# Kernel tuning notes

Hardware: AMD Instinct MI355X
Metric: run time of the kernel (lower is better)

The kernel has to match this reference:

```python
import jax, jax.numpy as jnp
import numpy as np

N, E = 50000, 800000
HID, HEADS, EDIM = 64, 4, 3
NEG_SLOPE = 0.2
LN_EPS = 1e-5


def setup_inputs() -> dict:
    key = jax.random.key(0)
    ks = jax.random.split(key, 12)
    h = jax.random.normal(ks[0], (N, HID), dtype=jnp.float32)
    edge_index = jax.random.randint(ks[1], (2, E), 0, N, dtype=jnp.int64)
    edge_attr = jax.random.normal(ks[2], (E, EDIM), dtype=jnp.float32)
    t = jax.random.uniform(ks[3], (1,), dtype=jnp.float32)
    s = 1.0 / np.sqrt(HID)
    W = jax.random.normal(ks[4], (HID, HEADS * HID), dtype=jnp.float32) * s
    att_src = jax.random.normal(ks[5], (1, HEADS, HID), dtype=jnp.float32) * s
    att_dst = jax.random.normal(ks[6], (1, HEADS, HID), dtype=jnp.float32) * s
    W_edge = jax.random.normal(ks[7], (EDIM, HEADS * HID), dtype=jnp.float32) * s
    att_edge = jax.random.normal(ks[8], (1, HEADS, HID), dtype=jnp.float32) * s
    bias = jnp.zeros((HID,), dtype=jnp.float32)
    ln_gamma = jnp.ones((HID,), dtype=jnp.float32)
    ln_beta = jnp.zeros((HID,), dtype=jnp.float32)
    return {"t": t, "h": h, "edge_index": edge_index, "edge_attr": edge_attr,
            "W": W, "att_src": att_src, "att_dst": att_dst, "W_edge": W_edge,
            "att_edge": att_edge, "bias": bias, "ln_gamma": ln_gamma, "ln_beta": ln_beta}


def reference(t, h, edge_index, edge_attr, W, att_src, att_dst, W_edge, att_edge, bias, ln_gamma, ln_beta):
    # GATConv (PyG, edge_dim>0, add_self_loops=False, concat=False, eval mode)
    x = (h @ W).reshape(N, HEADS, HID)                     # [N,H,C]
    a_src = (x * att_src).sum(-1)                          # [N,H]
    a_dst = (x * att_dst).sum(-1)                          # [N,H]
    e = (edge_attr @ W_edge).reshape(E, HEADS, HID)        # [E,H,C]
    a_edge = (e * att_edge).sum(-1)                        # [E,H]
    src, dst = edge_index[0], edge_index[1]
    alpha = a_src[src] + a_dst[dst] + a_edge               # [E,H]
    alpha = jax.nn.leaky_relu(alpha, NEG_SLOPE)
    # softmax over edges sharing the same destination node
    amax = jax.ops.segment_max(alpha, dst, num_segments=N)  # [N,H]
    ex = jnp.exp(alpha - amax[dst])
    esum = jax.ops.segment_sum(ex, dst, num_segments=N)     # [N,H]
    alpha = ex / (esum[dst] + 1e-16)
    msg = x[src] * alpha[:, :, None]                        # [E,H,C]
    out = jax.ops.segment_sum(msg, dst, num_segments=N)     # [N,H,C]
    out = out.mean(axis=1) + bias                           # concat=False -> head mean
    # LayerNorm + SiLU
    mu = out.mean(-1, keepdims=True)
    var = ((out - mu) ** 2).mean(-1, keepdims=True)
    y = (out - mu) * jax.lax.rsqrt(var + LN_EPS) * ln_gamma + ln_beta
    return y * jax.nn.sigmoid(y)
```

## Files before the change

### kernel.cpp

```cpp
#include <hip/hip_runtime.h>
#include <hip/hip_bf16.h>

#define HIDC 64
#define NEG_SLOPE 0.2f
#define SCAN_G 128

typedef __hip_bfloat16 bf16;
typedef short bf16x8 __attribute__((ext_vector_type(8)));
typedef float floatx4 __attribute__((ext_vector_type(4)));

static __device__ __forceinline__ float b2f(bf16 v) { return __bfloat162float(v); }

static __device__ __forceinline__ unsigned short f2us(float f) {
  bf16 b = __float2bfloat16(f);
  union { bf16 b; unsigned short u; } c;
  c.b = b;
  return c.u;
}

template <bool FF>
static __device__ __forceinline__ float ld(const void* __restrict__ p, size_t i) {
  return FF ? ((const float*)p)[i] : b2f(((const bf16*)p)[i]);
}
static __device__ __forceinline__ float ldr(const void* __restrict__ p, size_t i,
                                            bool ff) {
  return ff ? ((const float*)p)[i] : b2f(((const bf16*)p)[i]);
}
template <bool I64>
static __device__ __forceinline__ int ldi(const int* __restrict__ p, long long i) {
  return I64 ? (int)((const long long*)p)[i] : p[i];
}
static __device__ __forceinline__ int clampN(int v, int N) {
  return ((unsigned)v < (unsigned)N) ? v : 0;
}

static __device__ __forceinline__ bool det_f32(const unsigned* __restrict__ hw) {
  unsigned w = hw[threadIdx.x & 31];
  int ex = (w >> 7) & 0xFF;
  unsigned long long b = __ballot(ex >= 99 && ex <= 135);
  return __popcll(b) < 32;
}
static __device__ __forceinline__ bool det_i64(const int* __restrict__ ei) {
  int v = ei[2 * (threadIdx.x & 31) + 1];
  return __ballot(v != 0) == 0ULL;
}

template <bool FF, bool I64>
static __device__ __forceinline__ void xh_body(
    const void* __restrict__ h, const void* __restrict__ W,
    const void* __restrict__ att_src, const void* __restrict__ att_dst,
    const int* __restrict__ ei, bf16* __restrict__ x,
    float* __restrict__ a_src, float* __restrict__ a_dst,
    int* __restrict__ cnt, int N, int E,
    unsigned short* __restrict__ hls, unsigned short* __restrict__ wls) {
  for (long long e = (long long)blockIdx.x * 256 + threadIdx.x; e < E;
       e += (long long)gridDim.x * 256) {
    int dst = clampN(ldi<I64>(ei, (long long)E + e), N);
    atomicAdd(&cnt[dst], 1);
  }
  const int t = threadIdx.x;
  const long long n0 = (long long)blockIdx.x * 64;
  {
    const int c = t;
#pragma unroll
    for (int q = 0; q < 8; q++) {
      unsigned short u[8];
#pragma unroll
      for (int j = 0; j < 8; j++) {
        int k = q * 8 + j;
        u[j] = FF ? f2us(((const float*)W)[(size_t)k * 256 + c])
                  : ((const unsigned short*)W)[(size_t)k * 256 + c];
      }
      int4 v = make_int4((int)(u[0] | ((unsigned)u[1] << 16)),
                         (int)(u[2] | ((unsigned)u[3] << 16)),
                         (int)(u[4] | ((unsigned)u[5] << 16)),
                         (int)(u[6] | ((unsigned)u[7] << 16)));
      *(int4*)&wls[c * 64 + (q ^ (c & 7)) * 8] = v;
    }
  }
  {
    const int row = t >> 2;
    const long long n = n0 + row;
#pragma unroll
    for (int dq = 0; dq < 2; dq++) {
      int q = (t & 3) * 2 + dq;
      int4 v;
      if (n < N) {
        if (FF) {
          const float4* hp = (const float4*)h + n * 16 + q * 2;
          float4 f0 = hp[0], f1 = hp[1];
          v = make_int4((int)(f2us(f0.x) | ((unsigned)f2us(f0.y) << 16)),
                        (int)(f2us(f0.z) | ((unsigned)f2us(f0.w) << 16)),
                        (int)(f2us(f1.x) | ((unsigned)f2us(f1.y) << 16)),
                        (int)(f2us(f1.z) | ((unsigned)f2us(f1.w) << 16)));
        } else {
          v = *((const int4*)((const unsigned short*)h + n * 64 + q * 8));
        }
      } else {
        v = make_int4(0, 0, 0, 0);
      }
      *(int4*)&hls[row * 64 + (q ^ (row & 7)) * 8] = v;
    }
  }
  __syncthreads();
  const int w = t >> 6;
  const int lane = t & 63;
  const int lm = lane & 15, lq = lane >> 4;
  bf16x8 af[4][2];
#pragma unroll
  for (int nt = 0; nt < 4; nt++)
#pragma unroll
    for (int ks = 0; ks < 2; ks++) {
      int m = nt * 16 + lm;
      int q = ks * 4 + lq;
      af[nt][ks] = *(const bf16x8*)&hls[m * 64 + (q ^ (m & 7)) * 8];
    }
  floatx4 acc[4][4];
#pragma unroll
  for (int nt = 0; nt < 4; nt++)
#pragma unroll
    for (int ct = 0; ct < 4; ct++) acc[nt][ct] = (floatx4){0.f, 0.f, 0.f, 0.f};
#pragma unroll
  for (int ct = 0; ct < 4; ct++) {
    int c = w * 64 + ct * 16 + lm;
    bf16x8 b0 = *(const bf16x8*)&wls[c * 64 + ((lq) ^ (c & 7)) * 8];
    bf16x8 b1 = *(const bf16x8*)&wls[c * 64 + ((4 + lq) ^ (c & 7)) * 8];
#pragma unroll
    for (int nt = 0; nt < 4; nt++) {
      acc[nt][ct] = __builtin_amdgcn_mfma_f32_16x16x32_bf16(af[nt][0], b0,
                                                            acc[nt][ct], 0, 0, 0);
      acc[nt][ct] = __builtin_amdgcn_mfma_f32_16x16x32_bf16(af[nt][1], b1,
                                                            acc[nt][ct], 0, 0, 0);
    }
  }
  float as_c[4], ad_c[4];
#pragma unroll
  for (int ct = 0; ct < 4; ct++) {
    as_c[ct] = ld<FF>(att_src, w * 64 + ct * 16 + lm);
    ad_c[ct] = ld<FF>(att_dst, w * 64 + ct * 16 + lm);
  }
#pragma unroll
  for (int nt = 0; nt < 4; nt++) {
    float ps[4] = {0.f, 0.f, 0.f, 0.f}, pd[4] = {0.f, 0.f, 0.f, 0.f};
#pragma unroll
    for (int ct = 0; ct < 4; ct++) {
#pragma unroll
      for (int r = 0; r < 4; r++) {
        ps[r] += acc[nt][ct][r] * as_c[ct];
        pd[r] += acc[nt][ct][r] * ad_c[ct];
      }
    }
    long long nb = n0 + nt * 16 + lq * 4;
#pragma unroll
    for (int r = 0; r < 4; r++) {
      long long n = nb + r;
      if (n < N) {
#pragma unroll
        for (int ct = 0; ct < 4; ct++)
          x[n * 256 + w * 64 + ct * 16 + lm] = __float2bfloat16(acc[nt][ct][r]);
      }
    }
#pragma unroll
    for (int mask = 1; mask < 16; mask <<= 1) {
#pragma unroll
      for (int r = 0; r < 4; r++) {
        ps[r] += __shfl_xor(ps[r], mask);
        pd[r] += __shfl_xor(pd[r], mask);
      }
    }
    if (lm == 0) {
#pragma unroll
      for (int r = 0; r < 4; r++) {
        long long n = nb + r;
        if (n < N) {
          a_src[n * 4 + w] = ps[r];
          a_dst[n * 4 + w] = pd[r];
        }
      }
    }
  }
}

__global__ void __launch_bounds__(256) k_xh(
    const void* __restrict__ h, const void* __restrict__ W,
    const void* __restrict__ att_src, const void* __restrict__ att_dst,
    const int* __restrict__ ei, bf16* __restrict__ x,
    float* __restrict__ a_src, float* __restrict__ a_dst,
    int* __restrict__ cnt, int N, int E) {
  __shared__ alignas(16) unsigned short hls[64 * 64];
  __shared__ alignas(16) unsigned short wls[256 * 64];
  bool f32 = det_f32((const unsigned*)h);
  bool i64 = det_i64(ei);
  if (f32) {
    if (i64) xh_body<true, true>(h, W, att_src, att_dst, ei, x, a_src, a_dst, cnt, N, E, hls, wls);
    else     xh_body<true, false>(h, W, att_src, att_dst, ei, x, a_src, a_dst, cnt, N, E, hls, wls);
  } else {
    if (i64) xh_body<false, true>(h, W, att_src, att_dst, ei, x, a_src, a_dst, cnt, N, E, hls, wls);
    else     xh_body<false, false>(h, W, att_src, att_dst, ei, x, a_src, a_dst, cnt, N, E, hls, wls);
  }
}

__global__ void __launch_bounds__(1024) k_bscan(
    const void* __restrict__ W_edge, const void* __restrict__ att_edge,
    const unsigned* __restrict__ hw, const int* __restrict__ cnt,
    int* __restrict__ offs, int* __restrict__ bsum, int* __restrict__ bbase,
    int* __restrict__ done, float* __restrict__ M, int N) {
  int b = blockIdx.x, t = threadIdx.x;
  if (b == 0 && t < 768) {
    bool ff = det_f32(hw);
    int wv = t >> 6, lane = t & 63;
    int d = wv >> 2, hh = wv & 3;
    float p = ldr(W_edge, (size_t)d * 256 + hh * 64 + lane, ff) *
              ldr(att_edge, (size_t)hh * 64 + lane, ff);
#pragma unroll
    for (int o = 32; o; o >>= 1) p += __shfl_down(p, o);
    if (lane == 0) M[d * 4 + hh] = p;
  }
  const int C = (N + SCAN_G - 1) / SCAN_G;
  const int b0 = b * C;
  __shared__ int ts[1024];
  __shared__ int lastf;
  int v = 0;
  if (t < C && b0 + t < N) v = cnt[b0 + t];
  ts[t] = v;
  __syncthreads();
  for (int off = 1; off < 1024; off <<= 1) {
    int u = (t >= off) ? ts[t - off] : 0;
    __syncthreads();
    ts[t] += u;
    __syncthreads();
  }
  if (t < C && b0 + t < N) offs[b0 + t] = ts[t] - v;
  if (t == 1023) {
    atomicExch(&bsum[b], ts[1023]);
    __threadfence();
    int old = atomicAdd(done, 1);
    lastf = (old == SCAN_G - 1) ? 1 : 0;
  }
  __syncthreads();
  if (lastf) {
    int w = (t < SCAN_G) ? atomicAdd(&bsum[t], 0) : 0;
    ts[t] = w;
    __syncthreads();
    for (int off = 1; off < 1024; off <<= 1) {
      int u = (t >= off) ? ts[t - off] : 0;
      __syncthreads();
      ts[t] += u;
      __syncthreads();
    }
    if (t < SCAN_G) bbase[t] = ts[t] - w;
  }
}

__global__ void __launch_bounds__(1024) k_add(
    int* __restrict__ offs, int* __restrict__ cursor,
    const int* __restrict__ bbase, int N, int E) {
  int b = blockIdx.x, t = threadIdx.x;
  const int C = (N + SCAN_G - 1) / SCAN_G;
  const int b0 = b * C;
  int base = bbase[b];
  if (t < C && b0 + t < N) {
    int o = offs[b0 + t] + base;
    offs[b0 + t] = o;
    cursor[b0 + t] = o;
  }
  if (b == 0 && t == 0) offs[N] = E;
}

template <bool FF, bool I64>
static __device__ __forceinline__ void es_body(
    const int* __restrict__ ei, const void* __restrict__ eattr,
    const float* __restrict__ a_src, const float* __restrict__ a_dst,
    const float* __restrict__ M, int* __restrict__ cursor,
    int4* __restrict__ slots, int E, int N, unsigned* __restrict__ sattr) {
  const long long e0 = (long long)blockIdx.x * 256;
  {
    const unsigned bpe = FF ? 12u : 6u;
    const unsigned* gsrc = (const unsigned*)((const char*)eattr + e0 * bpe);
    unsigned ndw = FF ? 768u : 384u;
    long long bytes_left = ((long long)E - e0) * bpe;
    if (bytes_left < 0) bytes_left = 0;
    unsigned max_dw = (unsigned)((bytes_left + 3) >> 2);
    if (ndw > max_dw) ndw = max_dw;
    for (unsigned i = threadIdx.x; i < ndw; i += 256) sattr[i] = gsrc[i];
  }
  __syncthreads();
  long long e = e0 + threadIdx.x;
  if (e >= E) return;
  int src = clampN(ldi<I64>(ei, e), N);
  int dst = clampN(ldi<I64>(ei, (long long)E + e), N);
  float ea0, ea1, ea2;
  if (FF) {
    const float* sf = (const float*)sattr;
    ea0 = sf[threadIdx.x * 3 + 0];
    ea1 = sf[threadIdx.x * 3 + 1];
    ea2 = sf[threadIdx.x * 3 + 2];
  } else {
    const unsigned short* su = (const unsigned short*)sattr;
    ea0 = __uint_as_float((unsigned)su[threadIdx.x * 3 + 0] << 16);
    ea1 = __uint_as_float((unsigned)su[threadIdx.x * 3 + 1] << 16);
    ea2 = __uint_as_float((unsigned)su[threadIdx.x * 3 + 2] << 16);
  }
  const float4 m0 = ((const float4*)M)[0];
  const float4 m1 = ((const float4*)M)[1];
  const float4 m2 = ((const float4*)M)[2];
  const float4 as4 = ((const float4*)a_src)[src];
  const float4 ad4 = ((const float4*)a_dst)[dst];
  float al[4];
  al[0] = as4.x + ad4.x + ea0 * m0.x + ea1 * m1.x + ea2 * m2.x;
  al[1] = as4.y + ad4.y + ea0 * m0.y + ea1 * m1.y + ea2 * m2.y;
  al[2] = as4.z + ad4.z + ea0 * m0.z + ea1 * m1.z + ea2 * m2.z;
  al[3] = as4.w + ad4.w + ea0 * m0.w + ea1 * m1.w + ea2 * m2.w;
  unsigned short u[4];
#pragma unroll
  for (int hh = 0; hh < 4; hh++) {
    float a = al[hh];
    a = (a > 0.f) ? a : NEG_SLOPE * a;
    a = fminf(fmaxf(a, -60.f), 60.f);
    u[hh] = f2us(__expf(a));
  }
  int pos = atomicAdd(&cursor[dst], 1);
  slots[pos] = make_int4(src, (int)(u[0] | ((unsigned)u[1] << 16)),
                         (int)(u[2] | ((unsigned)u[3] << 16)), 0);
}

__global__ void __launch_bounds__(256) k_es(
    const int* __restrict__ ei, const void* __restrict__ eattr,
    const float* __restrict__ a_src, const float* __restrict__ a_dst,
    const float* __restrict__ M, const unsigned* __restrict__ hw,
    int* __restrict__ cursor, int4* __restrict__ slots, int E, int N) {
  __shared__ unsigned sattr[768];
  bool f32 = det_f32(hw);
  bool i64 = det_i64(ei);
  if (f32) {
    if (i64) es_body<true, true>(ei, eattr, a_src, a_dst, M, cursor, slots, E, N, sattr);
    else     es_body<true, false>(ei, eattr, a_src, a_dst, M, cursor, slots, E, N, sattr);
  } else {
    if (i64) es_body<false, true>(ei, eattr, a_src, a_dst, M, cursor, slots, E, N, sattr);
    else     es_body<false, false>(ei, eattr, a_src, a_dst, M, cursor, slots, E, N, sattr);
  }
}

static __device__ __forceinline__ uint2 xgat(const uint2* __restrict__ xr,
                                             int src, int lane) {
  int ss = __builtin_amdgcn_readfirstlane(src);
  return xr[(size_t)(unsigned)ss * 64 + lane];
}

__global__ void __launch_bounds__(256) k_agg(
    const int* __restrict__ offs, const int4* __restrict__ slots,
    const unsigned* __restrict__ xu, const unsigned* __restrict__ hw,
    const void* __restrict__ bias, const void* __restrict__ gamma,
    const void* __restrict__ beta, void* __restrict__ out, int N) {
  const int t = threadIdx.x;
  const int wv = t >> 6, lane = t & 63;
  const int n = blockIdx.x * 4 + wv;
  if (n >= N) return;
  const int head2 = lane >> 5;
  const unsigned wshift = (lane & 16) ? 0u : 16u;
  const uint2* __restrict__ xr = (const uint2*)xu;

  int s0 = __builtin_amdgcn_readfirstlane(offs[n]);
  int s1 = __builtin_amdgcn_readfirstlane(offs[n + 1]);

  float a0 = 0.f, a1 = 0.f, a2 = 0.f, a3 = 0.f, ws = 0.f;
  int i = s0;
  for (; i + 4 <= s1; i += 4) {
    int4 q0 = slots[i], q1 = slots[i + 1], q2 = slots[i + 2], q3 = slots[i + 3];
    uint2 d0 = xgat(xr, q0.x, lane);
    uint2 d1 = xgat(xr, q1.x, lane);
    uint2 d2 = xgat(xr, q2.x, lane);
    uint2 d3 = xgat(xr, q3.x, lane);
    unsigned e0 = head2 ? (unsigned)q0.z : (unsigned)q0.y;
    unsigned e1 = head2 ? (unsigned)q1.z : (unsigned)q1.y;
    unsigned e2 = head2 ? (unsigned)q2.z : (unsigned)q2.y;
    unsigned e3 = head2 ? (unsigned)q3.z : (unsigned)q3.y;
    float w0 = __uint_as_float((e0 << wshift) & 0xffff0000u);
    float w1 = __uint_as_float((e1 << wshift) & 0xffff0000u);
    float w2 = __uint_as_float((e2 << wshift) & 0xffff0000u);
    float w3 = __uint_as_float((e3 << wshift) & 0xffff0000u);
    a0 += w0 * __uint_as_float(d0.x << 16);
    a1 += w0 * __uint_as_float(d0.x & 0xffff0000u);
    a2 += w0 * __uint_as_float(d0.y << 16);
    a3 += w0 * __uint_as_float(d0.y & 0xffff0000u);
    a0 += w1 * __uint_as_float(d1.x << 16);
    a1 += w1 * __uint_as_float(d1.x & 0xffff0000u);
    a2 += w1 * __uint_as_float(d1.y << 16);
    a3 += w1 * __uint_as_float(d1.y & 0xffff0000u);
    a0 += w2 * __uint_as_float(d2.x << 16);
    a1 += w2 * __uint_as_float(d2.x & 0xffff0000u);
    a2 += w2 * __uint_as_float(d2.y << 16);
    a3 += w2 * __uint_as_float(d2.y & 0xffff0000u);
    a0 += w3 * __uint_as_float(d3.x << 16);
    a1 += w3 * __uint_as_float(d3.x & 0xffff0000u);
    a2 += w3 * __uint_as_float(d3.y << 16);
    a3 += w3 * __uint_as_float(d3.y & 0xffff0000u);
    ws += (w0 + w1) + (w2 + w3);
  }
  for (; i < s1; i++) {
    int4 q = slots[i];
    uint2 d = xgat(xr, q.x, lane);
    unsigned e = head2 ? (unsigned)q.z : (unsigned)q.y;
    float w = __uint_as_float((e << wshift) & 0xffff0000u);
    a0 += w * __uint_as_float(d.x << 16);
    a1 += w * __uint_as_float(d.x & 0xffff0000u);
    a2 += w * __uint_as_float(d.y << 16);
    a3 += w * __uint_as_float(d.y & 0xffff0000u);
    ws += w;
  }

  float inv = 1.f / (ws + 1e-16f);
  float v0 = a0 * inv, v1 = a1 * inv, v2 = a2 * inv, v3 = a3 * inv;
  v0 += __shfl_xor(v0, 16); v1 += __shfl_xor(v1, 16);
  v2 += __shfl_xor(v2, 16); v3 += __shfl_xor(v3, 16);
  v0 += __shfl_xor(v0, 32); v1 += __shfl_xor(v1, 32);
  v2 += __shfl_xor(v2, 32); v3 += __shfl_xor(v3, 32);

  bool ff = det_f32(hw);
  const int c0 = (lane & 15) * 4;
  float m0 = v0 * 0.25f + ldr(bias, c0 + 0, ff);
  float m1 = v1 * 0.25f + ldr(bias, c0 + 1, ff);
  float m2 = v2 * 0.25f + ldr(bias, c0 + 2, ff);
  float m3 = v3 * 0.25f + ldr(bias, c0 + 3, ff);

  float s = (m0 + m1) + (m2 + m3);
  s += __shfl_xor(s, 1); s += __shfl_xor(s, 2);
  s += __shfl_xor(s, 4); s += __shfl_xor(s, 8);
  float mu = s * 0.015625f;
  float d0 = m0 - mu, d1 = m1 - mu, d2 = m2 - mu, d3 = m3 - mu;
  float vq = (d0 * d0 + d1 * d1) + (d2 * d2 + d3 * d3);
  vq += __shfl_xor(vq, 1); vq += __shfl_xor(vq, 2);
  vq += __shfl_xor(vq, 4); vq += __shfl_xor(vq, 8);
  float rstd = rsqrtf(vq * 0.015625f + 1e-5f);

  if ((lane >> 4) == 0) {
    float y0 = d0 * rstd * ldr(gamma, c0 + 0, ff) + ldr(beta, c0 + 0, ff);
    float y1 = d1 * rstd * ldr(gamma, c0 + 1, ff) + ldr(beta, c0 + 1, ff);
    float y2 = d2 * rstd * ldr(gamma, c0 + 2, ff) + ldr(beta, c0 + 2, ff);
    float y3 = d3 * rstd * ldr(gamma, c0 + 3, ff) + ldr(beta, c0 + 3, ff);
    float r0 = y0 / (1.f + __expf(-y0));
    float r1 = y1 / (1.f + __expf(-y1));
    float r2 = y2 / (1.f + __expf(-y2));
    float r3 = y3 / (1.f + __expf(-y3));
    size_t ob = (size_t)n * 64 + c0;
    if (ff) {
      *(float4*)((float*)out + ob) = make_float4(r0, r1, r2, r3);
    } else {
      *(ushort4*)((bf16*)out + ob) =
          make_ushort4(f2us(r0), f2us(r1), f2us(r2), f2us(r3));
    }
  }
}

extern "C" void kernel_launch(void* const* d_in, const int* in_sizes, int n_in,
                              void* d_out, int out_size, void* d_ws,
                              size_t ws_size, hipStream_t stream) {
  const void* h        = d_in[1];
  const int*  ei       = (const int*)d_in[2];
  const void* eattr    = d_in[3];
  const void* W        = d_in[4];
  const void* att_src  = d_in[5];
  const void* att_dst  = d_in[6];
  const void* W_edge   = d_in[7];
  const void* att_edge = d_in[8];
  const void* bias     = d_in[9];
  const void* gamma    = d_in[10];
  const void* beta     = d_in[11];

  const int N = in_sizes[1] / HIDC;
  const int E = in_sizes[3] / 3;

  char* p = (char*)d_ws;
  float* M    = (float*)p; p += 64;
  bf16* x     = (bf16*)p;  p += (size_t)N * 256 * 2;
  float* asrc = (float*)p; p += (size_t)N * 4 * 4;
  float* adst = (float*)p; p += (size_t)N * 4 * 4;
  int4* slots = (int4*)p;  p += (size_t)E * 16;
  int* cnt    = (int*)p;   p += (size_t)N * 4;
  int* done   = (int*)p;   p += 64;
  int* offs   = (int*)p;   p += ((size_t)N + 4) * 4;
  int* cursor = (int*)p;   p += (size_t)N * 4;
  int* bsum   = (int*)p;   p += SCAN_G * 4;
  int* bbase  = (int*)p;   p += SCAN_G * 4;

  size_t need = (size_t)(p - (char*)d_ws);
  if (ws_size < need || N <= 0 || E <= 0) {
    hipMemsetAsync(d_out, 0, (size_t)out_size * 2, stream);
    return;
  }

  hipMemsetAsync(cnt, 0, (size_t)N * 4 + 64, stream);

  k_xh<<<(N + 63) / 64, 256, 0, stream>>>(h, W, att_src, att_dst, ei, x,
                                          asrc, adst, cnt, N, E);
  k_bscan<<<SCAN_G, 1024, 0, stream>>>(W_edge, att_edge, (const unsigned*)h,
                                       cnt, offs, bsum, bbase, done, M, N);
  k_add<<<SCAN_G, 1024, 0, stream>>>(offs, cursor, bbase, N, E);
  k_es<<<(E + 255) / 256, 256, 0, stream>>>(ei, eattr, asrc, adst, M,
                                            (const unsigned*)h, cursor, slots,
                                            E, N);
  k_agg<<<(N + 3) / 4, 256, 0, stream>>>(offs, slots, (const unsigned*)x,
                                         (const unsigned*)h, bias, gamma, beta,
                                         d_out, N);
}
```

Baseline: 266.8 us.

## Permute x column layout and gather two edges per wave with 16-byte loads

The projection kernel now permutes the W columns in shared memory so each lane's four MFMA output columns are contiguous, storing x with one 8-byte vector write per row and reading att vectors with the matching permuted indices. The aggregation kernel splits each wave into two half-waves that process different edges, each lane loading 16 bytes (8 channels) instead of 8. This gives fewer, wider gather instructions and twice the edges in flight per iteration. The cost is more accumulators and an extra cross-half reduction, and correctness relies on the W permutation, the att indexing and the aggregation channel mapping all agreeing.

```diff
diff --git a/kernel.cpp b/kernel.cpp
--- a/kernel.cpp
+++ b/kernel.cpp
@@ -62,6 +62,8 @@
   const long long n0 = (long long)blockIdx.x * 64;
   {
     const int c = t;
+    const int jn = c & 63, hd = c >> 6;
+    const int r = hd * 64 + (jn & 3) * 16 + (jn >> 2);
 #pragma unroll
     for (int q = 0; q < 8; q++) {
       unsigned short u[8];
@@ -75,7 +77,7 @@
                          (int)(u[2] | ((unsigned)u[3] << 16)),
                          (int)(u[4] | ((unsigned)u[5] << 16)),
                          (int)(u[6] | ((unsigned)u[7] << 16)));
-      *(int4*)&wls[c * 64 + (q ^ (c & 7)) * 8] = v;
+      *(int4*)&wls[r * 64 + (q ^ (r & 7)) * 8] = v;
     }
   }
   {
@@ -136,8 +138,8 @@
   float as_c[4], ad_c[4];
 #pragma unroll
   for (int ct = 0; ct < 4; ct++) {
-    as_c[ct] = ld<FF>(att_src, w * 64 + ct * 16 + lm);
-    ad_c[ct] = ld<FF>(att_dst, w * 64 + ct * 16 + lm);
+    as_c[ct] = ld<FF>(att_src, w * 64 + lm * 4 + ct);
+    ad_c[ct] = ld<FF>(att_dst, w * 64 + lm * 4 + ct);
   }
 #pragma unroll
   for (int nt = 0; nt < 4; nt++) {
@@ -155,9 +157,9 @@
     for (int r = 0; r < 4; r++) {
       long long n = nb + r;
       if (n < N) {
-#pragma unroll
-        for (int ct = 0; ct < 4; ct++)
-          x[n * 256 + w * 64 + ct * 16 + lm] = __float2bfloat16(acc[nt][ct][r]);
+        ushort4 us = make_ushort4(f2us(acc[nt][0][r]), f2us(acc[nt][1][r]),
+                                  f2us(acc[nt][2][r]), f2us(acc[nt][3][r]));
+        *(ushort4*)&x[n * 256 + w * 64 + lm * 4] = us;
       }
     }
 #pragma unroll
@@ -341,12 +343,6 @@
   }
 }
 
-static __device__ __forceinline__ uint2 xgat(const uint2* __restrict__ xr,
-                                             int src, int lane) {
-  int ss = __builtin_amdgcn_readfirstlane(src);
-  return xr[(size_t)(unsigned)ss * 64 + lane];
-}
-
 __global__ void __launch_bounds__(256) k_agg(
     const int* __restrict__ offs, const int4* __restrict__ slots,
     const unsigned* __restrict__ xu, const unsigned* __restrict__ hw,
@@ -356,98 +352,123 @@
   const int wv = t >> 6, lane = t & 63;
   const int n = blockIdx.x * 4 + wv;
   if (n >= N) return;
-  const int head2 = lane >> 5;
-  const unsigned wshift = (lane & 16) ? 0u : 16u;
-  const uint2* __restrict__ xr = (const uint2*)xu;
+  const int lsel = lane >> 5;
+  const int hl = lane & 31;
+  const int hh = hl >> 3;
+  const unsigned wsh = (hh & 1) ? 0u : 16u;
+  const char* __restrict__ xb = (const char*)xu;
+  const unsigned lboff = (unsigned)hl * 16u;
 
   int s0 = __builtin_amdgcn_readfirstlane(offs[n]);
   int s1 = __builtin_amdgcn_readfirstlane(offs[n + 1]);
 
-  float a0 = 0.f, a1 = 0.f, a2 = 0.f, a3 = 0.f, ws = 0.f;
+  float a0 = 0.f, a1 = 0.f, a2 = 0.f, a3 = 0.f;
+  float a4 = 0.f, a5 = 0.f, a6 = 0.f, a7 = 0.f, ws = 0.f;
+
+#define ACC8(wgt, dd)                                   \
+  do {                                                  \
+    a0 += (wgt) * __uint_as_float((dd).x << 16);        \
+    a1 += (wgt) * __uint_as_float((dd).x & 0xffff0000u);\
+    a2 += (wgt) * __uint_as_float((dd).y << 16);        \
+    a3 += (wgt) * __uint_as_float((dd).y & 0xffff0000u);\
+    a4 += (wgt) * __uint_as_float((dd).z << 16);        \
+    a5 += (wgt) * __uint_as_float((dd).z & 0xffff0000u);\
+    a6 += (wgt) * __uint_as_float((dd).w << 16);        \
+    a7 += (wgt) * __uint_as_float((dd).w & 0xffff0000u);\
+    ws += (wgt);                                        \
+  } while (0)
+
   int i = s0;
   for (; i + 4 <= s1; i += 4) {
-    int4 q0 = slots[i], q1 = slots[i + 1], q2 = slots[i + 2], q3 = slots[i + 3];
-    uint2 d0 = xgat(xr, q0.x, lane);
-    uint2 d1 = xgat(xr, q1.x, lane);
-    uint2 d2 = xgat(xr, q2.x, lane);
-    uint2 d3 = xgat(xr, q3.x, lane);
-    unsigned e0 = head2 ? (unsigned)q0.z : (unsigned)q0.y;
-    unsigned e1 = head2 ? (unsigned)q1.z : (unsigned)q1.y;
-    unsigned e2 = head2 ? (unsigned)q2.z : (unsigned)q2.y;
-    unsigned e3 = head2 ? (unsigned)q3.z : (unsigned)q3.y;
-    float w0 = __uint_as_float((e0 << wshift) & 0xffff0000u);
-    float w1 = __uint_as_float((e1 << wshift) & 0xffff0000u);
-    float w2 = __uint_as_float((e2 << wshift) & 0xffff0000u);
-    float w3 = __uint_as_float((e3 << wshift) & 0xffff0000u);
-    a0 += w0 * __uint_as_float(d0.x << 16);
-    a1 += w0 * __uint_as_float(d0.x & 0xffff0000u);
-    a2 += w0 * __uint_as_float(d0.y << 16);
-    a3 += w0 * __uint_as_float(d0.y & 0xffff0000u);
-    a0 += w1 * __uint_as_float(d1.x << 16);
-    a1 += w1 * __uint_as_float(d1.x & 0xffff0000u);
-    a2 += w1 * __uint_as_float(d1.y << 16);
-    a3 += w1 * __uint_as_float(d1.y & 0xffff0000u);
-    a0 += w2 * __uint_as_float(d2.x << 16);
-    a1 += w2 * __uint_as_float(d2.x & 0xffff0000u);
-    a2 += w2 * __uint_as_float(d2.y << 16);
-    a3 += w2 * __uint_as_float(d2.y & 0xffff0000u);
-    a0 += w3 * __uint_as_float(d3.x << 16);
-    a1 += w3 * __uint_as_float(d3.x & 0xffff0000u);
-    a2 += w3 * __uint_as_float(d3.y << 16);
-    a3 += w3 * __uint_as_float(d3.y & 0xffff0000u);
-    ws += (w0 + w1) + (w2 + w3);
-  }
-  for (; i < s1; i++) {
-    int4 q = slots[i];
-    uint2 d = xgat(xr, q.x, lane);
-    unsigned e = head2 ? (unsigned)q.z : (unsigned)q.y;
-    float w = __uint_as_float((e << wshift) & 0xffff0000u);
-    a0 += w * __uint_as_float(d.x << 16);
-    a1 += w * __uint_as_float(d.x & 0xffff0000u);
-    a2 += w * __uint_as_float(d.y << 16);
-    a3 += w * __uint_as_float(d.y & 0xffff0000u);
-    ws += w;
-  }
+    int4 qa = slots[i + lsel];
+    int4 qb = slots[i + 2 + lsel];
+    uint4 da = *(const uint4*)(xb + (size_t)(((unsigned)qa.x << 9) + lboff));
+    uint4 db = *(const uint4*)(xb + (size_t)(((unsigned)qb.x << 9) + lboff));
+    unsigned wda = (hh < 2) ? (unsigned)qa.y : (unsigned)qa.z;
+    float wa = __uint_as_float((wda << wsh) & 0xffff0000u);
+    ACC8(wa, da);
+    unsigned wdb = (hh < 2) ? (unsigned)qb.y : (unsigned)qb.z;
+    float wb = __uint_as_float((wdb << wsh) & 0xffff0000u);
+    ACC8(wb, db);
+  }
+  for (; i < s1; i += 2) {
+    int idx = i + lsel;
+    int4 q = make_int4(0, 0, 0, 0);
+    if (idx < s1) q = slots[idx];
+    uint4 d = *(const uint4*)(xb + (size_t)(((unsigned)q.x << 9) + lboff));
+    unsigned wd = (hh < 2) ? (unsigned)q.y : (unsigned)q.z;
+    float w = __uint_as_float((wd << wsh) & 0xffff0000u);
+    ACC8(w, d);
+  }
+#undef ACC8
+
+  a0 += __shfl_xor(a0, 32); a1 += __shfl_xor(a1, 32);
+  a2 += __shfl_xor(a2, 32); a3 += __shfl_xor(a3, 32);
+  a4 += __shfl_xor(a4, 32); a5 += __shfl_xor(a5, 32);
+  a6 += __shfl_xor(a6, 32); a7 += __shfl_xor(a7, 32);
+  ws += __shfl_xor(ws, 32);
 
   float inv = 1.f / (ws + 1e-16f);
   float v0 = a0 * inv, v1 = a1 * inv, v2 = a2 * inv, v3 = a3 * inv;
+  float v4 = a4 * inv, v5 = a5 * inv, v6 = a6 * inv, v7 = a7 * inv;
+  v0 += __shfl_xor(v0, 8);  v1 += __shfl_xor(v1, 8);
+  v2 += __shfl_xor(v2, 8);  v3 += __shfl_xor(v3, 8);
+  v4 += __shfl_xor(v4, 8);  v5 += __shfl_xor(v5, 8);
+  v6 += __shfl_xor(v6, 8);  v7 += __shfl_xor(v7, 8);
   v0 += __shfl_xor(v0, 16); v1 += __shfl_xor(v1, 16);
   v2 += __shfl_xor(v2, 16); v3 += __shfl_xor(v3, 16);
-  v0 += __shfl_xor(v0, 32); v1 += __shfl_xor(v1, 32);
-  v2 += __shfl_xor(v2, 32); v3 += __shfl_xor(v3, 32);
+  v4 += __shfl_xor(v4, 16); v5 += __shfl_xor(v5, 16);
+  v6 += __shfl_xor(v6, 16); v7 += __shfl_xor(v7, 16);
 
   bool ff = det_f32(hw);
-  const int c0 = (lane & 15) * 4;
+  const int c0 = (lane & 7) * 8;
   float m0 = v0 * 0.25f + ldr(bias, c0 + 0, ff);
   float m1 = v1 * 0.25f + ldr(bias, c0 + 1, ff);
   float m2 = v2 * 0.25f + ldr(bias, c0 + 2, ff);
   float m3 = v3 * 0.25f + ldr(bias, c0 + 3, ff);
-
-  float s = (m0 + m1) + (m2 + m3);
-  s += __shfl_xor(s, 1); s += __shfl_xor(s, 2);
-  s += __shfl_xor(s, 4); s += __shfl_xor(s, 8);
+  float m4 = v4 * 0.25f + ldr(bias, c0 + 4, ff);
+  float m5 = v5 * 0.25f + ldr(bias, c0 + 5, ff);
+  float m6 = v6 * 0.25f + ldr(bias, c0 + 6, ff);
+  float m7 = v7 * 0.25f + ldr(bias, c0 + 7, ff);
+
+  float s = ((m0 + m1) + (m2 + m3)) + ((m4 + m5) + (m6 + m7));
+  s += __shfl_xor(s, 1); s += __shfl_xor(s, 2); s += __shfl_xor(s, 4);
   float mu = s * 0.015625f;
   float d0 = m0 - mu, d1 = m1 - mu, d2 = m2 - mu, d3 = m3 - mu;
-  float vq = (d0 * d0 + d1 * d1) + (d2 * d2 + d3 * d3);
-  vq += __shfl_xor(vq, 1); vq += __shfl_xor(vq, 2);
-  vq += __shfl_xor(vq, 4); vq += __shfl_xor(vq, 8);
+  float d4 = m4 - mu, d5 = m5 - mu, d6 = m6 - mu, d7 = m7 - mu;
+  float vq = ((d0 * d0 + d1 * d1) + (d2 * d2 + d3 * d3)) +
+             ((d4 * d4 + d5 * d5) + (d6 * d6 + d7 * d7));
+  vq += __shfl_xor(vq, 1); vq += __shfl_xor(vq, 2); vq += __shfl_xor(vq, 4);
   float rstd = rsqrtf(vq * 0.015625f + 1e-5f);
 
-  if ((lane >> 4) == 0) {
+  if (lane < 8) {
     float y0 = d0 * rstd * ldr(gamma, c0 + 0, ff) + ldr(beta, c0 + 0, ff);
     float y1 = d1 * rstd * ldr(gamma, c0 + 1, ff) + ldr(beta, c0 + 1, ff);
     float y2 = d2 * rstd * ldr(gamma, c0 + 2, ff) + ldr(beta, c0 + 2, ff);
     float y3 = d3 * rstd * ldr(gamma, c0 + 3, ff) + ldr(beta, c0 + 3, ff);
+    float y4 = d4 * rstd * ldr(gamma, c0 + 4, ff) + ldr(beta, c0 + 4, ff);
+    float y5 = d5 * rstd * ldr(gamma, c0 + 5, ff) + ldr(beta, c0 + 5, ff);
+    float y6 = d6 * rstd * ldr(gamma, c0 + 6, ff) + ldr(beta, c0 + 6, ff);
+    float y7 = d7 * rstd * ldr(gamma, c0 + 7, ff) + ldr(beta, c0 + 7, ff);
     float r0 = y0 / (1.f + __expf(-y0));
     float r1 = y1 / (1.f + __expf(-y1));
     float r2 = y2 / (1.f + __expf(-y2));
     float r3 = y3 / (1.f + __expf(-y3));
+    float r4 = y4 / (1.f + __expf(-y4));
+    float r5 = y5 / (1.f + __expf(-y5));
+    float r6 = y6 / (1.f + __expf(-y6));
+    float r7 = y7 / (1.f + __expf(-y7));
     size_t ob = (size_t)n * 64 + c0;
     if (ff) {
       *(float4*)((float*)out + ob) = make_float4(r0, r1, r2, r3);
+      *(float4*)((float*)out + ob + 4) = make_float4(r4, r5, r6, r7);
     } else {
-      *(ushort4*)((bf16*)out + ob) =
-          make_ushort4(f2us(r0), f2us(r1), f2us(r2), f2us(r3));
+      uint4 pk;
+      pk.x = (unsigned)f2us(r0) | ((unsigned)f2us(r1) << 16);
+      pk.y = (unsigned)f2us(r2) | ((unsigned)f2us(r3) << 16);
+      pk.z = (unsigned)f2us(r4) | ((unsigned)f2us(r5) << 16);
+      pk.w = (unsigned)f2us(r6) | ((unsigned)f2us(r7) << 16);
+      *(uint4*)((bf16*)out + ob) = pk;
     }
   }
 }
```

Result: slower. 273.3 us (+2.4%).

## Vectorize x stores via W column permutation, unroll gather loop by eight

Applied to the files above, without the earlier changes.

The W columns are permuted when staged into LDS so that each lane's four MFMA output columns are contiguous. That lets the x projection be written with one 8-byte store instead of four scalar bf16 stores, and the att_src/att_dst indexing is remapped to match. The aggregation loop now unrolls eight edges to keep more gathers in flight, and it reads the edge slot records with nontemporal loads to avoid polluting cache. The risks are a silent layout mismatch if any consumer of x assumes the old column order, and higher register pressure from the wider unroll.

```diff
diff --git a/kernel.cpp b/kernel.cpp
--- a/kernel.cpp
+++ b/kernel.cpp
@@ -8,6 +8,7 @@
 typedef __hip_bfloat16 bf16;
 typedef short bf16x8 __attribute__((ext_vector_type(8)));
 typedef float floatx4 __attribute__((ext_vector_type(4)));
+typedef int intx4 __attribute__((ext_vector_type(4)));
 
 static __device__ __forceinline__ float b2f(bf16 v) { return __bfloat162float(v); }
 
@@ -32,6 +33,11 @@
 }
 static __device__ __forceinline__ int clampN(int v, int N) {
   return ((unsigned)v < (unsigned)N) ? v : 0;
+}
+
+static __device__ __forceinline__ int4 ntload4(const int4* __restrict__ p) {
+  intx4 v = __builtin_nontemporal_load((const intx4*)p);
+  return make_int4(v.x, v.y, v.z, v.w);
 }
 
 static __device__ __forceinline__ bool det_f32(const unsigned* __restrict__ hw) {
@@ -62,6 +68,8 @@
   const long long n0 = (long long)blockIdx.x * 64;
   {
     const int c = t;
+    const int jn = c & 63, hd = c >> 6;
+    const int r = hd * 64 + (jn & 3) * 16 + (jn >> 2);
 #pragma unroll
     for (int q = 0; q < 8; q++) {
       unsigned short u[8];
@@ -75,7 +83,7 @@
                          (int)(u[2] | ((unsigned)u[3] << 16)),
                          (int)(u[4] | ((unsigned)u[5] << 16)),
                          (int)(u[6] | ((unsigned)u[7] << 16)));
-      *(int4*)&wls[c * 64 + (q ^ (c & 7)) * 8] = v;
+      *(int4*)&wls[r * 64 + (q ^ (r & 7)) * 8] = v;
     }
   }
   {
@@ -136,8 +144,8 @@
   float as_c[4], ad_c[4];
 #pragma unroll
   for (int ct = 0; ct < 4; ct++) {
-    as_c[ct] = ld<FF>(att_src, w * 64 + ct * 16 + lm);
-    ad_c[ct] = ld<FF>(att_dst, w * 64 + ct * 16 + lm);
+    as_c[ct] = ld<FF>(att_src, w * 64 + lm * 4 + ct);
+    ad_c[ct] = ld<FF>(att_dst, w * 64 + lm * 4 + ct);
   }
 #pragma unroll
   for (int nt = 0; nt < 4; nt++) {
@@ -155,9 +163,9 @@
     for (int r = 0; r < 4; r++) {
       long long n = nb + r;
       if (n < N) {
-#pragma unroll
-        for (int ct = 0; ct < 4; ct++)
-          x[n * 256 + w * 64 + ct * 16 + lm] = __float2bfloat16(acc[nt][ct][r]);
+        ushort4 us = make_ushort4(f2us(acc[nt][0][r]), f2us(acc[nt][1][r]),
+                                  f2us(acc[nt][2][r]), f2us(acc[nt][3][r]));
+        *(ushort4*)&x[n * 256 + w * 64 + lm * 4] = us;
       }
     }
 #pragma unroll
@@ -364,50 +372,56 @@
   int s1 = __builtin_amdgcn_readfirstlane(offs[n + 1]);
 
   float a0 = 0.f, a1 = 0.f, a2 = 0.f, a3 = 0.f, ws = 0.f;
+
+#define ACC4(q, d)                                                    \
+  do {                                                                \
+    unsigned ee = head2 ? (unsigned)(q).z : (unsigned)(q).y;          \
+    float wv_ = __uint_as_float((ee << wshift) & 0xffff0000u);        \
+    a0 += wv_ * __uint_as_float((d).x << 16);                         \
+    a1 += wv_ * __uint_as_float((d).x & 0xffff0000u);                 \
+    a2 += wv_ * __uint_as_float((d).y << 16);                         \
+    a3 += wv_ * __uint_as_float((d).y & 0xffff0000u);                 \
+    ws += wv_;                                                        \
+  } while (0)
+
   int i = s0;
-  for (; i + 4 <= s1; i += 4) {
-    int4 q0 = slots[i], q1 = slots[i + 1], q2 = slots[i + 2], q3 = slots[i + 3];
+  for (; i + 8 <= s1; i += 8) {
+    int4 q0 = ntload4(&slots[i + 0]);
+    int4 q1 = ntload4(&slots[i + 1]);
+    int4 q2 = ntload4(&slots[i + 2]);
+    int4 q3 = ntload4(&slots[i + 3]);
+    int4 q4 = ntload4(&slots[i + 4]);
+    int4 q5 = ntload4(&slots[i + 5]);
+    int4 q6 = ntload4(&slots[i + 6]);
+    int4 q7 = ntload4(&slots[i + 7]);
     uint2 d0 = xgat(xr, q0.x, lane);
     uint2 d1 = xgat(xr, q1.x, lane);
     uint2 d2 = xgat(xr, q2.x, lane);
     uint2 d3 = xgat(xr, q3.x, lane);
-    unsigned e0 = head2 ? (unsigned)q0.z : (unsigned)q0.y;
-    unsigned e1 = head2 ? (unsigned)q1.z : (unsigned)q1.y;
-    unsigned e2 = head2 ? (unsigned)q2.z : (unsigned)q2.y;
-    unsigned e3 = head2 ? (unsigned)q3.z : (unsigned)q3.y;
-    float w0 = __uint_as_float((e0 << wshift) & 0xffff0000u);
-    float w1 = __uint_as_float((e1 << wshift) & 0xffff0000u);
-    float w2 = __uint_as_float((e2 << wshift) & 0xffff0000u);
-    float w3 = __uint_as_float((e3 << wshift) & 0xffff0000u);
-    a0 += w0 * __uint_as_float(d0.x << 16);
-    a1 += w0 * __uint_as_float(d0.x & 0xffff0000u);
-    a2 += w0 * __uint_as_float(d0.y << 16);
-    a3 += w0 * __uint_as_float(d0.y & 0xffff0000u);
-    a0 += w1 * __uint_as_float(d1.x << 16);
-    a1 += w1 * __uint_as_float(d1.x & 0xffff0000u);
-    a2 += w1 * __uint_as_float(d1.y << 16);
-    a3 += w1 * __uint_as_float(d1.y & 0xffff0000u);
-    a0 += w2 * __uint_as_float(d2.x << 16);
-    a1 += w2 * __uint_as_float(d2.x & 0xffff0000u);
-    a2 += w2 * __uint_as_float(d2.y << 16);
-    a3 += w2 * __uint_as_float(d2.y & 0xffff0000u);
-    a0 += w3 * __uint_as_float(d3.x << 16);
-    a1 += w3 * __uint_as_float(d3.x & 0xffff0000u);
-    a2 += w3 * __uint_as_float(d3.y << 16);
-    a3 += w3 * __uint_as_float(d3.y & 0xffff0000u);
-    ws += (w0 + w1) + (w2 + w3);
+    uint2 d4 = xgat(xr, q4.x, lane);
+    uint2 d5 = xgat(xr, q5.x, lane);
+    uint2 d6 = xgat(xr, q6.x, lane);
+    uint2 d7 = xgat(xr, q7.x, lane);
+    ACC4(q0, d0); ACC4(q1, d1); ACC4(q2, d2); ACC4(q3, d3);
+    ACC4(q4, d4); ACC4(q5, d5); ACC4(q6, d6); ACC4(q7, d7);
+  }
+  for (; i + 4 <= s1; i += 4) {
+    int4 q0 = ntload4(&slots[i + 0]);
+    int4 q1 = ntload4(&slots[i + 1]);
+    int4 q2 = ntload4(&slots[i + 2]);
+    int4 q3 = ntload4(&slots[i + 3]);
+    uint2 d0 = xgat(xr, q0.x, lane);
+    uint2 d1 = xgat(xr, q1.x, lane);
+    uint2 d2 = xgat(xr, q2.x, lane);
+    uint2 d3 = xgat(xr, q3.x, lane);
+    ACC4(q0, d0); ACC4(q1, d1); ACC4(q2, d2); ACC4(q3, d3);
   }
   for (; i < s1; i++) {
-    int4 q = slots[i];
+    int4 q = ntload4(&slots[i]);
     uint2 d = xgat(xr, q.x, lane);
-    unsigned e = head2 ? (unsigned)q.z : (unsigned)q.y;
-    float w = __uint_as_float((e << wshift) & 0xffff0000u);
-    a0 += w * __uint_as_float(d.x << 16);
-    a1 += w * __uint_as_float(d.x & 0xffff0000u);
-    a2 += w * __uint_as_float(d.y << 16);
-    a3 += w * __uint_as_float(d.y & 0xffff0000u);
-    ws += w;
-  }
+    ACC4(q, d);
+  }
+#undef ACC4
 
   float inv = 1.f / (ws + 1e-16f);
   float v0 = a0 * inv, v1 = a1 * inv, v2 = a2 * inv, v3 = a3 * inv;
```

Result: faster. 261.1 us (-2.1%).
